# Kernel tuning notes

Measured on AMD Instinct MI355X. Metric: run time of the kernel, lower is better.

Reference implementation:

```python
import jax, jax.numpy as jnp
import numpy as np
from jax import lax

NUM_CLASSES = 21
MAX_OUT = 5          # max_output_size in tf.image.non_max_suppression
IOU_THR = 0.5        # NMS_IOU_THRESHOLD
CONF_THR = 0.5       # CONFIDENCE_THRESHOLD
NEG = -1e9           # stand-in for -inf score (suppressed / background)


def setup_inputs() -> dict:
    key = jax.random.key(0)
    k1, k2, k3 = jax.random.split(key, 3)
    B, N, C = 128, 8732, NUM_CLASSES
    logits = jax.random.normal(k1, (B, N, 4 + C), dtype=jnp.float32)
    # default boxes in corner format [ymin, xmin, ymax, xmax], valid geometry
    ctr = jax.random.uniform(k2, (N, 2), dtype=jnp.float32)                 # cy, cx
    sz = jax.random.uniform(k3, (N, 2), dtype=jnp.float32, minval=0.05, maxval=0.3)  # h, w
    default_boxes = jnp.clip(
        jnp.concatenate([ctr - sz / 2, ctr + sz / 2], axis=-1), 0.0, 1.0)
    return {"logits": logits, "default_boxes": default_boxes}


def _decode(loc, db):
    # db: [N,4] corners -> center/size (matches get_offset's tf.stack)
    cy = (db[:, 2] + db[:, 0]) / 2
    cx = (db[:, 3] + db[:, 1]) / 2
    h = db[:, 2] - db[:, 0]
    w = db[:, 3] - db[:, 1]
    # loc: [B,N,4] = (dy, dx, dh, dw)
    ncy = loc[..., 0] * h + cy
    ncx = loc[..., 1] * w + cx
    nh = jnp.exp(loc[..., 2]) * h
    nw = jnp.exp(loc[..., 3]) * w
    boxes = jnp.stack(
        [ncy - nh / 2, ncx - nw / 2, ncy + nh / 2, ncx + nw / 2], axis=-1)
    return jnp.clip(boxes, 0.0, 1.0)


def _iou_one_vs_all(box, boxes):
    # box [4], boxes [N,4], corner format
    tl = jnp.maximum(box[:2], boxes[:, :2])
    br = jnp.minimum(box[2:], boxes[:, 2:])
    wh = jnp.maximum(br - tl, 0.0)
    inter = wh[:, 0] * wh[:, 1]
    a1 = (box[2] - box[0]) * (box[3] - box[1])
    a2 = (boxes[:, 2] - boxes[:, 0]) * (boxes[:, 3] - boxes[:, 1])
    return inter / (a1 + a2 - inter + 1e-12)


def _nms_single(boxes, scores, classes_f):
    # boxes [N,4], scores [N] (background already set to NEG), classes_f [N] float
    def step(s, _):
        i = jnp.argmax(s)
        sc = s[i]
        b = boxes[i]
        valid = sc > CONF_THR  # score_threshold in tf NMS
        iou = _iou_one_vs_all(b, boxes)
        s = jnp.where(iou > IOU_THR, NEG, s)  # suppresses i too (IoU=1)
        return s, (b, classes_f[i], sc, valid)

    _, (bs, cs, ss, vs) = lax.scan(step, scores, None, length=MAX_OUT)
    # pad invalid slots with zeros (TF returns variable-length; we use fixed 5 + zero pad)
    bs = jnp.where(vs[:, None], bs, 0.0)
    cs = jnp.where(vs, cs, 0.0)
    ss = jnp.where(vs, ss, 0.0)
    return bs, cs[:, None], ss[:, None]  # [5,4], [5,1], [5,1]


def reference(logits, default_boxes):
    boxes = _decode(logits[..., :4], default_boxes)          # [B,N,4]
    probs = jax.nn.softmax(logits[..., 4:], axis=-1)         # [B,N,C]
    scores = jnp.max(probs, axis=-1)                          # [B,N]
    classes = jnp.argmax(probs, axis=-1)                      # [B,N] int
    # boolean_mask(classes != 0) expressed as score = -inf for background
    scores_eff = jnp.where(classes != 0, scores, NEG)
    det_b, det_c, det_s = jax.vmap(_nms_single)(
        boxes, scores_eff, classes.astype(jnp.float32))
    # pack detection_boxes / detection_classes / detection_scores -> [B,5,6]
    return jnp.concatenate([det_b, det_c, det_s], axis=-1)
```

## Files before the change

kernel.cpp:

```cpp
#include <hip/hip_runtime.h>

#define NEG (-1e9f)
constexpr int NCLS  = 21;
constexpr int NBOX  = 8732;
constexpr int MAXOUT = 5;
constexpr float IOU_THR  = 0.5f;
constexpr float CONF_THR = 0.5f;

__global__ void decode_kernel(const float* __restrict__ logits,
                              const float* __restrict__ dbox,
                              float4* __restrict__ boxes,
                              float*  __restrict__ scores,
                              float*  __restrict__ cls,
                              int BN) {
    int i = blockIdx.x * blockDim.x + threadIdx.x;
    if (i >= BN) return;
    int n = i % NBOX;
    const float* L = logits + (long long)i * (4 + NCLS);

    float d0 = dbox[n * 4 + 0], d1 = dbox[n * 4 + 1];
    float d2 = dbox[n * 4 + 2], d3 = dbox[n * 4 + 3];
    float cy = (d2 + d0) * 0.5f;
    float cx = (d3 + d1) * 0.5f;
    float h  = d2 - d0;
    float w  = d3 - d1;
    float l0 = L[0], l1 = L[1], l2 = L[2], l3 = L[3];
    float ncy = l0 * h + cy;
    float ncx = l1 * w + cx;
    float nh  = expf(l2) * h;
    float nw  = expf(l3) * w;
    float y1 = fminf(fmaxf(ncy - nh * 0.5f, 0.f), 1.f);
    float x1 = fminf(fmaxf(ncx - nw * 0.5f, 0.f), 1.f);
    float y2 = fminf(fmaxf(ncy + nh * 0.5f, 0.f), 1.f);
    float x2 = fminf(fmaxf(ncx + nw * 0.5f, 0.f), 1.f);
    boxes[i] = make_float4(y1, x1, y2, x2);

    float m = L[4];
    int am = 0;
#pragma unroll
    for (int j = 1; j < NCLS; j++) {
        float x = L[4 + j];
        if (x > m) { m = x; am = j; }
    }
    float sum = 0.f;
#pragma unroll
    for (int j = 0; j < NCLS; j++) sum += expf(L[4 + j] - m);
    float score = 1.0f / sum;

    scores[i] = (am != 0) ? score : NEG;
    cls[i]    = (float)am;
}

__global__ __launch_bounds__(256) void nms_kernel(const float4* __restrict__ boxes,
                                                  const float*  __restrict__ scores,
                                                  const float*  __restrict__ cls,
                                                  float* __restrict__ out) {
    const int b = blockIdx.x;
    const int t = threadIdx.x;
    __shared__ float s_sc[NBOX];
    __shared__ float r_val[256];
    __shared__ int   r_idx[256];
    __shared__ float sel_box[4];

    const float4* bb = boxes  + (long long)b * NBOX;
    const float*  ss = scores + (long long)b * NBOX;

    for (int i = t; i < NBOX; i += 256) s_sc[i] = ss[i];
    __syncthreads();

    for (int k = 0; k < MAXOUT; k++) {
        float bv = -INFINITY;
        int   bi = NBOX;
        for (int i = t; i < NBOX; i += 256) {
            float v = s_sc[i];
            if (v > bv) { bv = v; bi = i; }
        }
        r_val[t] = bv; r_idx[t] = bi;
        __syncthreads();
        for (int off = 128; off > 0; off >>= 1) {
            if (t < off) {
                float v2 = r_val[t + off]; int i2 = r_idx[t + off];
                if (v2 > r_val[t] || (v2 == r_val[t] && i2 < r_idx[t])) {
                    r_val[t] = v2; r_idx[t] = i2;
                }
            }
            __syncthreads();
        }
        int   sel = r_idx[0];
        float sc  = r_val[0];

        if (t == 0) {
            float4 bx = bb[sel];
            sel_box[0] = bx.x; sel_box[1] = bx.y;
            sel_box[2] = bx.z; sel_box[3] = bx.w;
            float* o = out + ((long long)b * MAXOUT + k) * 6;
            bool valid = sc > CONF_THR;
            if (valid) {
                o[0] = bx.x; o[1] = bx.y; o[2] = bx.z; o[3] = bx.w;
                o[4] = cls[(long long)b * NBOX + sel];
                o[5] = sc;
            } else {
                o[0] = 0.f; o[1] = 0.f; o[2] = 0.f;
                o[3] = 0.f; o[4] = 0.f; o[5] = 0.f;
            }
        }
        __syncthreads();

        float by1 = sel_box[0], bx1 = sel_box[1];
        float by2 = sel_box[2], bx2 = sel_box[3];
        float a1 = (by2 - by1) * (bx2 - bx1);
        for (int i = t; i < NBOX; i += 256) {
            float4 c = bb[i];
            float tly = fmaxf(by1, c.x);
            float tlx = fmaxf(bx1, c.y);
            float bry = fminf(by2, c.z);
            float brx = fminf(bx2, c.w);
            float wh0 = fmaxf(bry - tly, 0.f);
            float wh1 = fmaxf(brx - tlx, 0.f);
            float inter = wh0 * wh1;
            float a2 = (c.z - c.x) * (c.w - c.y);
            float iou = inter / (a1 + a2 - inter + 1e-12f);
            if (iou > IOU_THR) s_sc[i] = NEG;
        }
        __syncthreads();
    }
}

extern "C" void kernel_launch(void* const* d_in, const int* in_sizes, int n_in,
                              void* d_out, int out_size, void* d_ws, size_t ws_size,
                              hipStream_t stream) {
    const float* logits = (const float*)d_in[0];
    const float* dbox   = (const float*)d_in[1];
    float* out          = (float*)d_out;

    const int N  = in_sizes[1] / 4;
    const int B  = in_sizes[0] / (N * 25);
    const int BN = B * N;

    float4* ws_boxes  = (float4*)d_ws;
    float*  ws_scores = (float*)((char*)d_ws + (size_t)BN * sizeof(float4));
    float*  ws_cls    = ws_scores + BN;

    decode_kernel<<<(BN + 255) / 256, 256, 0, stream>>>(
        logits, dbox, ws_boxes, ws_scores, ws_cls, BN);
    nms_kernel<<<B, 256, 0, stream>>>(ws_boxes, ws_scores, ws_cls, out);
}
```

Before: 208.0 us.

## Compact candidates above confidence threshold before NMS and stage logits in shared memory

The decode kernel now stages each block's logits through shared memory with float4 coalesced loads. It writes only boxes whose score passes the confidence threshold and is non-background, using a per-batch atomic counter, into a compact candidate list. NMS then scans only these candidates, breaking ties on the original index, and skips suppression once no valid box remains. This cuts the workspace writes and the NMS scan work, at the cost of an extra memset, global atomics and a tail-handling risk in the vector load.

```diff
diff --git a/kernel.cpp b/kernel.cpp
--- a/kernel.cpp
+++ b/kernel.cpp
@@ -1,22 +1,36 @@
 #include <hip/hip_runtime.h>
 
 #define NEG (-1e9f)
-constexpr int NCLS  = 21;
-constexpr int NBOX  = 8732;
+constexpr int NCLS   = 21;
+constexpr int NBOX   = 8732;
 constexpr int MAXOUT = 5;
+constexpr int CAP    = NBOX;
 constexpr float IOU_THR  = 0.5f;
 constexpr float CONF_THR = 0.5f;
 
-__global__ void decode_kernel(const float* __restrict__ logits,
-                              const float* __restrict__ dbox,
-                              float4* __restrict__ boxes,
-                              float*  __restrict__ scores,
-                              float*  __restrict__ cls,
-                              int BN) {
-    int i = blockIdx.x * blockDim.x + threadIdx.x;
+__global__ __launch_bounds__(256) void decode_kernel(
+        const float* __restrict__ logits,
+        const float* __restrict__ dbox,
+        float4* __restrict__ cand,
+        int* __restrict__ cnt,
+        int BN) {
+    __shared__ float sl[256 * 25];
+    const int t = threadIdx.x;
+    const long long baseF = (long long)blockIdx.x * (256 * 25);
+    const long long totalF = (long long)BN * 25;
+
+    const float4* gl = (const float4*)(logits + baseF);
+    float4* sl4 = (float4*)sl;
+    for (int j = t; j < 1600; j += 256) {
+        if (baseF + (long long)j * 4 + 3 < totalF) sl4[j] = gl[j];
+    }
+    __syncthreads();
+
+    const int i = blockIdx.x * 256 + t;
     if (i >= BN) return;
-    int n = i % NBOX;
-    const float* L = logits + (long long)i * (4 + NCLS);
+    const float* L = sl + t * 25;
+    const int n = i % NBOX;
+    const int b = i / NBOX;
 
     float d0 = dbox[n * 4 + 0], d1 = dbox[n * 4 + 1];
     float d2 = dbox[n * 4 + 2], d3 = dbox[n * 4 + 3];
@@ -24,16 +38,14 @@
     float cx = (d3 + d1) * 0.5f;
     float h  = d2 - d0;
     float w  = d3 - d1;
-    float l0 = L[0], l1 = L[1], l2 = L[2], l3 = L[3];
-    float ncy = l0 * h + cy;
-    float ncx = l1 * w + cx;
-    float nh  = expf(l2) * h;
-    float nw  = expf(l3) * w;
+    float ncy = L[0] * h + cy;
+    float ncx = L[1] * w + cx;
+    float nh  = expf(L[2]) * h;
+    float nw  = expf(L[3]) * w;
     float y1 = fminf(fmaxf(ncy - nh * 0.5f, 0.f), 1.f);
     float x1 = fminf(fmaxf(ncx - nw * 0.5f, 0.f), 1.f);
     float y2 = fminf(fmaxf(ncy + nh * 0.5f, 0.f), 1.f);
     float x2 = fminf(fmaxf(ncx + nw * 0.5f, 0.f), 1.f);
-    boxes[i] = make_float4(y1, x1, y2, x2);
 
     float m = L[4];
     int am = 0;
@@ -47,74 +59,85 @@
     for (int j = 0; j < NCLS; j++) sum += expf(L[4 + j] - m);
     float score = 1.0f / sum;
 
-    scores[i] = (am != 0) ? score : NEG;
-    cls[i]    = (float)am;
+    if (am != 0 && score > CONF_THR) {
+        int p = atomicAdd(&cnt[b], 1);
+        if (p < CAP) {
+            float4* c = cand + ((long long)b * CAP + p) * 2;
+            c[0] = make_float4(y1, x1, y2, x2);
+            c[1] = make_float4(score, (float)am, (float)n, 0.f);
+        }
+    }
 }
 
-__global__ __launch_bounds__(256) void nms_kernel(const float4* __restrict__ boxes,
-                                                  const float*  __restrict__ scores,
-                                                  const float*  __restrict__ cls,
-                                                  float* __restrict__ out) {
+__global__ __launch_bounds__(256) void nms_kernel(
+        const float4* __restrict__ cand,
+        const int* __restrict__ cnt,
+        float* __restrict__ out) {
     const int b = blockIdx.x;
     const int t = threadIdx.x;
-    __shared__ float s_sc[NBOX];
-    __shared__ float r_val[256];
-    __shared__ int   r_idx[256];
-    __shared__ float sel_box[4];
+    __shared__ float s_sc[CAP];
+    __shared__ float s_id[CAP];
+    __shared__ float r_v[256];
+    __shared__ float r_oid[256];
+    __shared__ int   r_i[256];
+    __shared__ float4 selbox_sh;
 
-    const float4* bb = boxes  + (long long)b * NBOX;
-    const float*  ss = scores + (long long)b * NBOX;
+    const int M = min(cnt[b], CAP);
+    const float4* cb = cand + (long long)b * CAP * 2;
 
-    for (int i = t; i < NBOX; i += 256) s_sc[i] = ss[i];
+    for (int i = t; i < M; i += 256) {
+        float4 mrec = cb[i * 2 + 1];
+        s_sc[i] = mrec.x;
+        s_id[i] = mrec.z;
+    }
     __syncthreads();
 
     for (int k = 0; k < MAXOUT; k++) {
-        float bv = -INFINITY;
-        int   bi = NBOX;
-        for (int i = t; i < NBOX; i += 256) {
-            float v = s_sc[i];
-            if (v > bv) { bv = v; bi = i; }
+        float bv = -INFINITY, boid = 3.0e38f;
+        int bi = -1;
+        for (int i = t; i < M; i += 256) {
+            float v = s_sc[i], oid = s_id[i];
+            if (v > bv || (v == bv && oid < boid)) { bv = v; boid = oid; bi = i; }
         }
-        r_val[t] = bv; r_idx[t] = bi;
+        r_v[t] = bv; r_oid[t] = boid; r_i[t] = bi;
         __syncthreads();
         for (int off = 128; off > 0; off >>= 1) {
             if (t < off) {
-                float v2 = r_val[t + off]; int i2 = r_idx[t + off];
-                if (v2 > r_val[t] || (v2 == r_val[t] && i2 < r_idx[t])) {
-                    r_val[t] = v2; r_idx[t] = i2;
+                float v2 = r_v[t + off];
+                if (v2 > r_v[t] || (v2 == r_v[t] && r_oid[t + off] < r_oid[t])) {
+                    r_v[t] = v2; r_oid[t] = r_oid[t + off]; r_i[t] = r_i[t + off];
                 }
             }
             __syncthreads();
         }
-        int   sel = r_idx[0];
-        float sc  = r_val[0];
+        const int   sel = r_i[0];
+        const float sc  = r_v[0];
+        const bool valid = (sel >= 0) && (sc > CONF_THR);
 
         if (t == 0) {
-            float4 bx = bb[sel];
-            sel_box[0] = bx.x; sel_box[1] = bx.y;
-            sel_box[2] = bx.z; sel_box[3] = bx.w;
             float* o = out + ((long long)b * MAXOUT + k) * 6;
-            bool valid = sc > CONF_THR;
             if (valid) {
+                float4 bx = cb[sel * 2];
+                float4 mm = cb[sel * 2 + 1];
+                selbox_sh = bx;
                 o[0] = bx.x; o[1] = bx.y; o[2] = bx.z; o[3] = bx.w;
-                o[4] = cls[(long long)b * NBOX + sel];
-                o[5] = sc;
+                o[4] = mm.y; o[5] = sc;
             } else {
                 o[0] = 0.f; o[1] = 0.f; o[2] = 0.f;
                 o[3] = 0.f; o[4] = 0.f; o[5] = 0.f;
             }
         }
         __syncthreads();
+        if (!valid) continue;
 
-        float by1 = sel_box[0], bx1 = sel_box[1];
-        float by2 = sel_box[2], bx2 = sel_box[3];
-        float a1 = (by2 - by1) * (bx2 - bx1);
-        for (int i = t; i < NBOX; i += 256) {
-            float4 c = bb[i];
-            float tly = fmaxf(by1, c.x);
-            float tlx = fmaxf(bx1, c.y);
-            float bry = fminf(by2, c.z);
-            float brx = fminf(bx2, c.w);
+        float4 sb = selbox_sh;
+        float a1 = (sb.z - sb.x) * (sb.w - sb.y);
+        for (int i = t; i < M; i += 256) {
+            float4 c = cb[i * 2];
+            float tly = fmaxf(sb.x, c.x);
+            float tlx = fmaxf(sb.y, c.y);
+            float bry = fminf(sb.z, c.z);
+            float brx = fminf(sb.w, c.w);
             float wh0 = fmaxf(bry - tly, 0.f);
             float wh1 = fmaxf(brx - tlx, 0.f);
             float inter = wh0 * wh1;
@@ -137,11 +160,10 @@
     const int B  = in_sizes[0] / (N * 25);
     const int BN = B * N;
 
-    float4* ws_boxes  = (float4*)d_ws;
-    float*  ws_scores = (float*)((char*)d_ws + (size_t)BN * sizeof(float4));
-    float*  ws_cls    = ws_scores + BN;
+    int* cnt = (int*)d_ws;
+    float4* cand = (float4*)((char*)d_ws + (((size_t)B * sizeof(int) + 15) & ~(size_t)15));
 
-    decode_kernel<<<(BN + 255) / 256, 256, 0, stream>>>(
-        logits, dbox, ws_boxes, ws_scores, ws_cls, BN);
-    nms_kernel<<<B, 256, 0, stream>>>(ws_boxes, ws_scores, ws_cls, out);
+    hipMemsetAsync(cnt, 0, (size_t)B * sizeof(int), stream);
+    decode_kernel<<<(BN + 255) / 256, 256, 0, stream>>>(logits, dbox, cand, cnt, BN);
+    nms_kernel<<<B, 256, 0, stream>>>(cand, cnt, out);
 }
```

After: 207.0 us. About the same (-0.5%).
